# Kernel tuning notes

Measured on AMD Instinct MI355X. Metric: run time of the kernel, lower is better.

## Reference

```python
import jax, jax.numpy as jnp
import numpy as np

NUM_HEADS = 4
NUM_GROUPS = 8
EPS = 1e-5


def group_norm(x, gamma, beta):
    B, C, H, W = x.shape
    xg = x.reshape(B, NUM_GROUPS, C // NUM_GROUPS, H, W)
    mean = xg.mean(axis=(2, 3, 4), keepdims=True)
    var = xg.var(axis=(2, 3, 4), keepdims=True)
    xn = ((xg - mean) * jax.lax.rsqrt(var + EPS)).reshape(B, C, H, W)
    return xn * gamma[None, :, None, None] + beta[None, :, None, None]


def setup_inputs() -> dict:
    key = jax.random.key(0)
    k1, k2, k3 = jax.random.split(key, 3)
    B, C, H, W = 16, 512, 32, 32
    x = jax.random.normal(k1, (B, C, H, W), dtype=jnp.float32)
    gn_gamma = jnp.ones((C,), dtype=jnp.float32)
    gn_beta = jnp.zeros((C,), dtype=jnp.float32)
    w_qkv = jax.random.normal(k2, (3 * C, C), dtype=jnp.float32) * 0.02
    w_proj = jax.random.normal(k3, (C, C), dtype=jnp.float32) * 0.02
    b_proj = jnp.zeros((C,), dtype=jnp.float32)
    return {"x": x, "gn_gamma": gn_gamma, "gn_beta": gn_beta,
            "w_qkv": w_qkv, "w_proj": w_proj, "b_proj": b_proj}


def reference(x, gn_gamma, gn_beta, w_qkv, w_proj, b_proj):
    B, C, H, W = x.shape
    nh = NUM_HEADS
    hd = C // nh
    N = H * W

    x_norm = group_norm(x, gn_gamma, gn_beta)
    # 1x1 conv == channel matmul: (B,C,H,W) x (3C,C) -> (B,3C,H,W)
    qkv = jnp.einsum('bchw,dc->bdhw', x_norm, w_qkv)
    qkv = qkv.reshape(B, 3, nh, hd, N)
    q, k, v = qkv[:, 0], qkv[:, 1], qkv[:, 2]  # each (B, nh, hd, N)

    scale = hd ** (-0.5)
    attn = jnp.einsum('bhci,bhcj->bhij', q, k) * scale  # (B, nh, N, N)
    attn = jax.nn.softmax(attn, axis=-1)
    out = jnp.einsum('bhij,bhcj->bhci', attn, v)  # (B, nh, hd, N)
    out = out.reshape(B, C, H, W)

    proj = jnp.einsum('bchw,dc->bdhw', out, w_proj) + b_proj[None, :, None, None]
    return x + proj
```

## Files before the change

kernel.cpp:

```cpp
#include <hip/hip_runtime.h>
#include <stdint.h>

typedef unsigned char u8;
typedef unsigned short u16;
typedef unsigned int u32;
typedef long long i64;
typedef __attribute__((ext_vector_type(8))) short short8;
typedef __attribute__((ext_vector_type(4))) float f32x4;
typedef __attribute__((ext_vector_type(16))) float f32x16;

#define BATCH 16
#define CCH   512
#define NPIX  1024
#define NGRP  8
#define CPG   64
#define NHEAD 4
#define HDIM  128

__device__ __forceinline__ u16 f2bf(float f) {
  union { float f; u32 u; } v; v.f = f;
  u32 u = v.u;
  u32 r = (u + 0x7FFFu + ((u >> 16) & 1u)) >> 16;
  return (u16)r;
}
__device__ __forceinline__ u8 f2fp8(float f) {
  return (u8)(__builtin_amdgcn_cvt_pk_fp8_f32(f, 0.f, 0, false) & 0xff);
}
__device__ __forceinline__ u32 pack4_fp8(float a, float b, float c, float d) {
  u32 w = (u32)__builtin_amdgcn_cvt_pk_fp8_f32(a, b, 0, false);
  w = (u32)__builtin_amdgcn_cvt_pk_fp8_f32(c, d, (int)w, true);
  return w;
}

__device__ __forceinline__ void gload16(const void* g, void* l) {
  typedef __attribute__((address_space(3))) u32 L;
  typedef __attribute__((address_space(1))) const u32 G;
  __builtin_amdgcn_global_load_lds((G*)(uintptr_t)g, (L*)(u32)(uintptr_t)l, 16, 0, 0);
}

#define PLSWAP(a, b) asm("v_permlane32_swap_b32 %0, %1" : "+v"(a), "+v"(b))

__device__ __forceinline__ short8 rd512(const char* base, int r, int ck, int hi) {
  int byte = ((r >> 2) * 512) +
             ((((r & 3) * 128) + ck * 32 + hi * 16) ^ (((r >> 2) & 15) << 4));
  return *reinterpret_cast<const short8*>(base + byte);
}

__global__ void gn_stats_k(const float* __restrict__ x, float* __restrict__ part) {
  int bg = blockIdx.x >> 3, sl = blockIdx.x & 7;
  const float* p = x + (size_t)bg * (CPG * NPIX) + sl * 8192;
  float s = 0.f, ss = 0.f;
  for (int i = threadIdx.x; i < 2048; i += 256) {
    float4 v = reinterpret_cast<const float4*>(p)[i];
    s  += v.x + v.y + v.z + v.w;
    ss += v.x*v.x + v.y*v.y + v.z*v.z + v.w*v.w;
  }
  for (int o = 32; o > 0; o >>= 1) { s += __shfl_down(s, o); ss += __shfl_down(ss, o); }
  __shared__ float sh[8];
  int wid = threadIdx.x >> 6;
  if ((threadIdx.x & 63) == 0) { sh[wid*2] = s; sh[wid*2+1] = ss; }
  __syncthreads();
  if (threadIdx.x == 0) {
    part[blockIdx.x*2]   = sh[0]+sh[2]+sh[4]+sh[6];
    part[blockIdx.x*2+1] = sh[1]+sh[3]+sh[5]+sh[7];
  }
}

__global__ __launch_bounds__(256) void gn_apply_t(const float* __restrict__ x,
                                                  const float* __restrict__ gamma,
                                                  const float* __restrict__ beta,
                                                  const float* __restrict__ part,
                                                  u16* __restrict__ xnT) {
  const int p0 = blockIdx.x * 64;
  const int c0 = blockIdx.y * 64;
  const int b  = blockIdx.z;
  __shared__ float lt[64][66];

  const int bg = b * NGRP + (c0 >> 6);
  float s = 0.f, ss = 0.f;
  #pragma unroll
  for (int k2 = 0; k2 < 8; ++k2) { s += part[(bg*8 + k2)*2]; ss += part[(bg*8 + k2)*2 + 1]; }
  const float invn = 1.f / (float)(CPG * NPIX);
  const float mean = s * invn;
  const float rstd = rsqrtf(ss * invn - mean * mean + 1e-5f);

  const int t = threadIdx.x;
  #pragma unroll
  for (int pass = 0; pass < 4; ++pass) {
    int c   = c0 + (t >> 4) + pass * 16;
    int pix = p0 + (t & 15) * 4;
    float ga = gamma[c] * rstd;
    float be = beta[c] - mean * ga;
    float4 v = *reinterpret_cast<const float4*>(&x[((size_t)(b*CCH + c)) * NPIX + pix]);
    int pl = (t & 15) * 4, cl = (t >> 4) + pass * 16;
    lt[pl+0][cl] = v.x*ga + be;
    lt[pl+1][cl] = v.y*ga + be;
    lt[pl+2][cl] = v.z*ga + be;
    lt[pl+3][cl] = v.w*ga + be;
  }
  __syncthreads();
  const int pl = t >> 2, cq = (t & 3) * 16;
  u32 wbuf[8];
  #pragma unroll
  for (int e = 0; e < 8; ++e) {
    u16 lo = f2bf(lt[pl][cq + e*2]);
    u16 hi = f2bf(lt[pl][cq + e*2 + 1]);
    wbuf[e] = (u32)lo | ((u32)hi << 16);
  }
  u32* dst = (u32*)&xnT[((size_t)(b*NPIX + p0 + pl)) * CCH + c0 + cq];
  #pragma unroll
  for (int e = 0; e < 8; ++e) dst[e] = wbuf[e];
}

__global__ void f2bf_all(const float* __restrict__ wqkv, const float* __restrict__ wproj,
                         u16* __restrict__ wq, u16* __restrict__ wp) {
  int i = blockIdx.x * 256 + threadIdx.x;
  float4 v; u16* dst;
  if (i < 196608) {
    v = reinterpret_cast<const float4*>(wqkv)[i];
    dst = wq + (size_t)i * 4;
  } else {
    v = reinterpret_cast<const float4*>(wproj)[i - 196608];
    dst = wp + (size_t)(i - 196608) * 4;
  }
  u32 lo = (u32)f2bf(v.x) | ((u32)f2bf(v.y) << 16);
  u32 hi = (u32)f2bf(v.z) | ((u32)f2bf(v.w) << 16);
  *reinterpret_cast<uint2*>(dst) = make_uint2(lo, hi);
}

__global__ __launch_bounds__(256, 2) void gemm_qkv(const u16* __restrict__ xnT,
                                                   const u16* __restrict__ wq_bf,
                                                   u8* __restrict__ outQ,
                                                   u8* __restrict__ outK,
                                                   u8* __restrict__ outV) {
  __shared__ __align__(16) char smem[65536];

  const int id = blockIdx.x;
  const int wg = (id & 7) * 192 + (id >> 3);
  const bool mode0 = (wg < 1024);
  int rt, ct;
  if (mode0) { rt = wg >> 3; ct = wg & 7; }
  else       { int w1 = wg - 1024; rt = w1 & 3; ct = w1 >> 2; }

  const char* Ab = mode0 ? (const char*)xnT + (size_t)rt * 131072
                         : (const char*)wq_bf + (size_t)(8 + rt) * 131072;
  const char* Bb = mode0 ? (const char*)wq_bf + (size_t)ct * 131072
                         : (const char*)xnT + (size_t)ct * 131072;

  const int t = threadIdx.x;
  const int lane = t & 63, w = t >> 6;
  const int q = lane & 31, hi = lane >> 5;
  const int rh = (w >> 1) * 64, ch = (w & 1) * 64;

  int soff[4];
  #pragma unroll
  for (int i = 0; i < 4; ++i) {
    int p = w*4096 + i*1024 + lane*16;
    int lrow = p >> 9, off = p & 511;
    int loff = off ^ ((lrow & 15) << 4);
    soff[i] = (lrow*4 + (loff >> 7)) * 1024 + (loff & 127);
  }

  #pragma unroll
  for (int i = 0; i < 4; ++i) {
    gload16(Ab + soff[i], smem +         w*4096 + i*1024);
    gload16(Bb + soff[i], smem + 16384 + w*4096 + i*1024);
  }

  f32x16 acc[2][2] = {};

  for (int kt = 0; kt < 8; ++kt) {
    asm volatile("s_waitcnt vmcnt(0)" ::: "memory");
    __syncthreads();
    const char* cur = smem + (kt & 1) * 32768;
    if (kt + 1 < 8) {
      char* nxt = smem + ((kt + 1) & 1) * 32768;
      #pragma unroll
      for (int i = 0; i < 4; ++i) {
        gload16(Ab + (kt+1)*128 + soff[i], nxt +         w*4096 + i*1024);
        gload16(Bb + (kt+1)*128 + soff[i], nxt + 16384 + w*4096 + i*1024);
      }
    }
    __builtin_amdgcn_s_setprio(1);
    #pragma unroll
    for (int ck = 0; ck < 4; ++ck) {
      short8 af0 = rd512(cur,         rh + q,      ck, hi);
      short8 af1 = rd512(cur,         rh + 32 + q, ck, hi);
      short8 bf0 = rd512(cur + 16384, ch + q,      ck, hi);
      short8 bf1 = rd512(cur + 16384, ch + 32 + q, ck, hi);
      acc[0][0] = __builtin_amdgcn_mfma_f32_32x32x16_bf16(af0, bf0, acc[0][0], 0, 0, 0);
      acc[0][1] = __builtin_amdgcn_mfma_f32_32x32x16_bf16(af0, bf1, acc[0][1], 0, 0, 0);
      acc[1][0] = __builtin_amdgcn_mfma_f32_32x32x16_bf16(af1, bf0, acc[1][0], 0, 0, 0);
      acc[1][1] = __builtin_amdgcn_mfma_f32_32x32x16_bf16(af1, bf1, acc[1][1], 0, 0, 0);
    }
    __builtin_amdgcn_s_setprio(0);
  }

  __syncthreads();
  u8* Dt = (u8*)smem;
  #pragma unroll
  for (int r = 0; r < 16; ++r) {
    int ar = (r & 3) + 8*(r >> 2) + 4*hi;
    Dt[(rh +      ar) * 144 + ch +      q] = f2fp8(acc[0][0][r]);
    Dt[(rh +      ar) * 144 + ch + 32 + q] = f2fp8(acc[0][1][r]);
    Dt[(rh + 32 + ar) * 144 + ch +      q] = f2fp8(acc[1][0][r]);
    Dt[(rh + 32 + ar) * 144 + ch + 32 + q] = f2fp8(acc[1][1][r]);
  }
  __syncthreads();

  const int rl = t >> 1, hoff = (t & 1) * 64;
  uint4 buf[4];
  const uint4* s4 = reinterpret_cast<const uint4*>(&Dt[rl*144 + hoff]);
  #pragma unroll
  for (int e = 0; e < 4; ++e) buf[e] = s4[e];

  u8* gdst;
  if (mode0) {
    const int tok0 = rt * 128;
    const int b = tok0 >> 10, pix0 = tok0 & 1023;
    const int h = ct & 3;
    u8* base = (ct >= 4) ? outK : outQ;
    gdst = base + ((size_t)((b*NHEAD + h)) * NPIX + pix0 + rl) * HDIM + hoff;
  } else {
    const int m0 = rt * 128, tok0 = ct * 128;
    const int b = tok0 >> 10, pix0 = tok0 & 1023;
    gdst = outV + ((size_t)(b*CCH + m0 + rl)) * NPIX + pix0 + hoff;
  }
  uint4* g4 = reinterpret_cast<uint4*>(gdst);
  #pragma unroll
  for (int e = 0; e < 4; ++e) g4[e] = buf[e];
}

__global__ __launch_bounds__(256, 2) void gemm_proj(const u16* __restrict__ wp_bf,
                                                    const u16* __restrict__ attnO,
                                                    const float* __restrict__ xres,
                                                    const float* __restrict__ bias,
                                                    float* __restrict__ outF) {
  __shared__ __align__(16) char smem[65536];

  const int id = blockIdx.x;
  const int wg = (id & 7) * 64 + (id >> 3);
  const int rt = wg & 3, ct = wg >> 2;

  const char* Ab = (const char*)wp_bf + (size_t)rt * 131072;
  const char* Bb = (const char*)attnO + (size_t)ct * 131072;

  const int t = threadIdx.x;
  const int lane = t & 63, w = t >> 6;
  const int q = lane & 31, hi = lane >> 5;
  const int rh = (w >> 1) * 64, ch = (w & 1) * 64;

  int soff[4];
  #pragma unroll
  for (int i = 0; i < 4; ++i) {
    int p = w*4096 + i*1024 + lane*16;
    int lrow = p >> 9, off = p & 511;
    int loff = off ^ ((lrow & 15) << 4);
    soff[i] = (lrow*4 + (loff >> 7)) * 1024 + (loff & 127);
  }

  #pragma unroll
  for (int i = 0; i < 4; ++i) {
    gload16(Ab + soff[i], smem +         w*4096 + i*1024);
    gload16(Bb + soff[i], smem + 16384 + w*4096 + i*1024);
  }

  f32x16 acc[2][2] = {};

  for (int kt = 0; kt < 8; ++kt) {
    asm volatile("s_waitcnt vmcnt(0)" ::: "memory");
    __syncthreads();
    const char* cur = smem + (kt & 1) * 32768;
    if (kt + 1 < 8) {
      char* nxt = smem + ((kt + 1) & 1) * 32768;
      #pragma unroll
      for (int i = 0; i < 4; ++i) {
        gload16(Ab + (kt+1)*128 + soff[i], nxt +         w*4096 + i*1024);
        gload16(Bb + (kt+1)*128 + soff[i], nxt + 16384 + w*4096 + i*1024);
      }
    }
    __builtin_amdgcn_s_setprio(1);
    #pragma unroll
    for (int ck = 0; ck < 4; ++ck) {
      short8 af0 = rd512(cur,         rh + q,      ck, hi);
      short8 af1 = rd512(cur,         rh + 32 + q, ck, hi);
      short8 bf0 = rd512(cur + 16384, ch + q,      ck, hi);
      short8 bf1 = rd512(cur + 16384, ch + 32 + q, ck, hi);
      acc[0][0] = __builtin_amdgcn_mfma_f32_32x32x16_bf16(af0, bf0, acc[0][0], 0, 0, 0);
      acc[0][1] = __builtin_amdgcn_mfma_f32_32x32x16_bf16(af0, bf1, acc[0][1], 0, 0, 0);
      acc[1][0] = __builtin_amdgcn_mfma_f32_32x32x16_bf16(af1, bf0, acc[1][0], 0, 0, 0);
      acc[1][1] = __builtin_amdgcn_mfma_f32_32x32x16_bf16(af1, bf1, acc[1][1], 0, 0, 0);
    }
    __builtin_amdgcn_s_setprio(0);
  }

  const int m0 = rt * 128, tok0 = ct * 128;
  const int b = tok0 >> 10, pix0 = tok0 & 1023;
  #pragma unroll
  for (int r = 0; r < 16; ++r) {
    int ar = (r & 3) + 8*(r >> 2) + 4*hi;
    int m0r = m0 + rh + ar, m1r = m0 + rh + 32 + ar;
    size_t o00 = ((size_t)(b*CCH + m0r)) * NPIX + pix0 + ch + q;
    size_t o01 = o00 + 32;
    size_t o10 = ((size_t)(b*CCH + m1r)) * NPIX + pix0 + ch + q;
    size_t o11 = o10 + 32;
    outF[o00] = xres[o00] + acc[0][0][r] + bias[m0r];
    outF[o01] = xres[o01] + acc[0][1][r] + bias[m0r];
    outF[o10] = xres[o10] + acc[1][0][r] + bias[m1r];
    outF[o11] = xres[o11] + acc[1][1][r] + bias[m1r];
  }
}

__global__ __launch_bounds__(256, 2) void attn_k(const u8* __restrict__ Qt,
                                                 const u8* __restrict__ Kt,
                                                 const u8* __restrict__ Vb,
                                                 u16* __restrict__ attnO) {
  int id = blockIdx.x;
  int swz = (id & 7) * 64 + (id >> 3);
  const int qt = swz & 7;
  const int h  = (swz >> 3) & 3;
  const int b  = swz >> 5;
  const int bh = b * NHEAD + h;

  __shared__ __align__(16) char smem[32768];

  const int t = threadIdx.x;
  const int lane = t & 63, w = t >> 6;
  const int q = lane & 31, hi = lane >> 5;

  const u8*   Qb    = Qt + ((size_t)bh * NPIX + qt*128 + w*32 + q) * HDIM;
  const char* Kbase = (const char*)Kt + (size_t)bh * NPIX * HDIM;
  const char* Vbase = (const char*)Vb + ((size_t)b*CCH + h*HDIM) * NPIX;

  i64 qf[8];
  #pragma unroll
  for (int ck = 0; ck < 8; ++ck)
    qf[ck] = *reinterpret_cast<const i64*>(Qb + ck*16 + hi*8);

  int koff[2], voff[2];
  #pragma unroll
  for (int i = 0; i < 2; ++i) {
    int d = i*4096 + w*1024 + lane*16;
    int r = d >> 7, x = d & 127;
    koff[i] = r*128 + (x ^ ((r & 15) << 3));
    int vc = 2*r + (x >> 6);
    voff[i] = vc*1024 + ((x & 63) ^ ((r & 7) << 3));
  }

  const int ksw = (q & 15) << 3;

  f32x16 of[4] = {};
  float l_run = 0.f;
  i64 pf[4];
  const float qs2 = 0.08838834764831845f * 1.44269504088896f;

  #pragma unroll
  for (int i = 0; i < 2; ++i)
    gload16(Kbase + koff[i],        smem +        i*4096 + w*1024);
  #pragma unroll
  for (int i = 0; i < 2; ++i)
    gload16(Kbase + 8192 + koff[i], smem + 8192 + i*4096 + w*1024);
  #pragma unroll
  for (int i = 0; i < 2; ++i)
    gload16(Vbase + voff[i],        smem + 16384 + i*4096 + w*1024);
  asm volatile("s_waitcnt vmcnt(0)" ::: "memory");
  __syncthreads();

  {
    f32x16 sn0 = {}, sn1 = {};
    #pragma unroll
    for (int ck = 0; ck < 8; ++ck) {
      const i64 kf0 = *reinterpret_cast<const i64*>(smem + q*128      + ((ck*16 + hi*8) ^ ksw));
      const i64 kf1 = *reinterpret_cast<const i64*>(smem + (32+q)*128 + ((ck*16 + hi*8) ^ ksw));
      sn0 = __builtin_amdgcn_mfma_f32_32x32x16_fp8_fp8(kf0, qf[ck], sn0, 0, 0, 0);
      sn1 = __builtin_amdgcn_mfma_f32_32x32x16_fp8_fp8(kf1, qf[ck], sn1, 0, 0, 0);
    }
    float ps = 0.f;
    float p[16];
    #pragma unroll
    for (int g = 0; g < 2; ++g) {
      const f32x16& sn = g ? sn1 : sn0;
      #pragma unroll
      for (int r = 0; r < 16; ++r) { p[r] = exp2f(sn[r] * qs2); ps += p[r]; }
      u32 pkl0 = pack4_fp8(p[0], p[1], p[2], p[3]);
      u32 pkh0 = pack4_fp8(p[4], p[5], p[6], p[7]);
      u32 pkl1 = pack4_fp8(p[8], p[9], p[10], p[11]);
      u32 pkh1 = pack4_fp8(p[12], p[13], p[14], p[15]);
      PLSWAP(pkl0, pkh0);
      PLSWAP(pkl1, pkh1);
      pf[g*2]   = (i64)(((unsigned long long)pkh0 << 32) | pkl0);
      pf[g*2+1] = (i64)(((unsigned long long)pkh1 << 32) | pkl1);
    }
    ps += __shfl_xor(ps, 32);
    l_run += ps;
  }

  for (int tt = 0; tt < 16; ++tt) {
    asm volatile("s_waitcnt vmcnt(2)" ::: "memory");
    __builtin_amdgcn_s_barrier();

    const char* kcur = smem + (((tt+1) & 1) << 13);
    const char* vcur = smem + 16384 + ((tt & 1) << 13);

    if (tt + 2 < 16) {
      char* kd = smem + ((tt & 1) << 13);
      #pragma unroll
      for (int i = 0; i < 2; ++i)
        gload16(Kbase + (size_t)(tt+2)*8192 + koff[i], kd + i*4096 + w*1024);
    }
    if (tt + 1 < 16) {
      char* vd = smem + 16384 + (((tt+1) & 1) << 13);
      #pragma unroll
      for (int i = 0; i < 2; ++i)
        gload16(Vbase + (size_t)(tt+1)*64 + voff[i], vd + i*4096 + w*1024);
    }

    f32x16 sn0 = {}, sn1 = {};
    __builtin_amdgcn_s_setprio(1);
    if (tt + 1 < 16) {
      #pragma unroll
      for (int ck = 0; ck < 8; ++ck) {
        const i64 kf0 = *reinterpret_cast<const i64*>(kcur + q*128      + ((ck*16 + hi*8) ^ ksw));
        const i64 kf1 = *reinterpret_cast<const i64*>(kcur + (32+q)*128 + ((ck*16 + hi*8) ^ ksw));
        sn0 = __builtin_amdgcn_mfma_f32_32x32x16_fp8_fp8(kf0, qf[ck], sn0, 0, 0, 0);
        sn1 = __builtin_amdgcn_mfma_f32_32x32x16_fp8_fp8(kf1, qf[ck], sn1, 0, 0, 0);
      }
    }
    __builtin_amdgcn_s_setprio(0);

    if (tt < 14)       asm volatile("s_waitcnt vmcnt(4)" ::: "memory");
    else if (tt == 14) asm volatile("s_waitcnt vmcnt(2)" ::: "memory");
    else               asm volatile("s_waitcnt vmcnt(0)" ::: "memory");
    __builtin_amdgcn_s_barrier();

    __builtin_amdgcn_s_setprio(1);
    #pragma unroll
    for (int cg = 0; cg < 4; ++cg) {
      const int c = cg*32 + q;
      const char* vrow = vcur + (c >> 1)*128 + (c & 1)*64;
      const int vsw = ((c >> 1) & 7) << 3;
      #pragma unroll
      for (int kc = 0; kc < 4; ++kc) {
        const i64 vf = *reinterpret_cast<const i64*>(vrow + ((kc*16 + hi*8) ^ vsw));
        of[cg] = __builtin_amdgcn_mfma_f32_32x32x16_fp8_fp8(vf, pf[kc], of[cg], 0, 0, 0);
      }
    }
    __builtin_amdgcn_s_setprio(0);

    if (tt + 1 < 16) {
      float ps = 0.f;
      float p[16];
      #pragma unroll
      for (int g = 0; g < 2; ++g) {
        const f32x16& sn = g ? sn1 : sn0;
        #pragma unroll
        for (int r = 0; r < 16; ++r) { p[r] = exp2f(sn[r] * qs2); ps += p[r]; }
        u32 pkl0 = pack4_fp8(p[0], p[1], p[2], p[3]);
        u32 pkh0 = pack4_fp8(p[4], p[5], p[6], p[7]);
        u32 pkl1 = pack4_fp8(p[8], p[9], p[10], p[11]);
        u32 pkh1 = pack4_fp8(p[12], p[13], p[14], p[15]);
        PLSWAP(pkl0, pkh0);
        PLSWAP(pkl1, pkh1);
        pf[g*2]   = (i64)(((unsigned long long)pkh0 << 32) | pkl0);
        pf[g*2+1] = (i64)(((unsigned long long)pkh1 << 32) | pkl1);
      }
      ps += __shfl_xor(ps, 32);
      l_run += ps;
    }
  }

  float inv = 1.f / l_run;
  u16* orow = attnO + ((size_t)(b*NPIX + qt*128 + w*32 + q)) * CCH + h*HDIM;
  #pragma unroll
  for (int cg = 0; cg < 4; ++cg) {
    #pragma unroll
    for (int u = 0; u < 8; ++u) {
      int c = cg*32 + ((2*u) & 3) + 8*(u >> 1) + 4*hi;
      u32 pk = (u32)f2bf(of[cg][2*u] * inv) | ((u32)f2bf(of[cg][2*u+1] * inv) << 16);
      *reinterpret_cast<u32*>(&orow[c]) = pk;
    }
  }
}

extern "C" void kernel_launch(void* const* d_in, const int* in_sizes, int n_in,
                              void* d_out, int out_size, void* d_ws, size_t ws_size,
                              hipStream_t stream) {
  const float* x     = (const float*)d_in[0];
  const float* gamma = (const float*)d_in[1];
  const float* beta  = (const float*)d_in[2];
  const float* wqkv  = (const float*)d_in[3];
  const float* wproj = (const float*)d_in[4];
  const float* bproj = (const float*)d_in[5];
  float* out = (float*)d_out;

  char* ws = (char*)d_ws;
  float* part   = (float*)ws;
  u16*   xnT    = (u16*)(ws + 8192);
  u16*   wq_bf  = (u16*)(ws + 8192 + (16u<<20));
  u16*   wp_bf  = (u16*)((char*)wq_bf + 1572864);
  u8*    Qt     = (u8*)((char*)wp_bf + 524288);
  u8*    Kt     = (u8*)((char*)Qt + (8u<<20));
  u8*    Vb     = (u8*)((char*)Kt + (8u<<20));
  u16*   attnO  = (u16*)((char*)Vb + (8u<<20));

  gn_stats_k<<<dim3(1024), dim3(256), 0, stream>>>(x, part);
  gn_apply_t<<<dim3(16, 8, BATCH), dim3(256), 0, stream>>>(x, gamma, beta, part, xnT);
  f2bf_all<<<dim3(1024), dim3(256), 0, stream>>>(wqkv, wproj, wq_bf, wp_bf);

  gemm_qkv<<<dim3(1536), dim3(256), 0, stream>>>(xnT, wq_bf, Qt, Kt, Vb);

  attn_k<<<dim3(512), dim3(256), 0, stream>>>(Qt, Kt, Vb, attnO);

  gemm_proj<<<dim3(512), dim3(256), 0, stream>>>(wp_bf, attnO, x, bproj, out);
}
```

Measured before the change: 114.1 us.

## Double attention KV tile to 128 keys and fuse weight conversion into stats kernel

The attention kernel now processes 128 keys per iteration instead of 64, doubling LDS to 64KB, halving the loop trip count and barrier count, and reading V in a new row-swizzled layout. The separate weight fp32-to-bf16 conversion kernel is merged into the group-norm stats kernel as extra blocks, removing one launch. The larger LDS footprint and extra score registers may lower occupancy below the two blocks per CU requested. The new V offset mapping must match how gemm_qkv writes V, and the diff does not show that writer being changed.

```diff
diff --git a/kernel.cpp b/kernel.cpp
--- a/kernel.cpp
+++ b/kernel.cpp
@@ -46,7 +46,25 @@
   return *reinterpret_cast<const short8*>(base + byte);
 }
 
-__global__ void gn_stats_k(const float* __restrict__ x, float* __restrict__ part) {
+__global__ void gn_stats_wconv(const float* __restrict__ x, float* __restrict__ part,
+                               const float* __restrict__ wqkv, const float* __restrict__ wproj,
+                               u16* __restrict__ wq, u16* __restrict__ wp) {
+  __shared__ float sh[8];
+  if (blockIdx.x >= 1024) {
+    int i = (blockIdx.x - 1024) * 256 + threadIdx.x;
+    float4 v; u16* dst;
+    if (i < 196608) {
+      v = reinterpret_cast<const float4*>(wqkv)[i];
+      dst = wq + (size_t)i * 4;
+    } else {
+      v = reinterpret_cast<const float4*>(wproj)[i - 196608];
+      dst = wp + (size_t)(i - 196608) * 4;
+    }
+    u32 lo = (u32)f2bf(v.x) | ((u32)f2bf(v.y) << 16);
+    u32 hi = (u32)f2bf(v.z) | ((u32)f2bf(v.w) << 16);
+    *reinterpret_cast<uint2*>(dst) = make_uint2(lo, hi);
+    return;
+  }
   int bg = blockIdx.x >> 3, sl = blockIdx.x & 7;
   const float* p = x + (size_t)bg * (CPG * NPIX) + sl * 8192;
   float s = 0.f, ss = 0.f;
@@ -56,7 +74,6 @@
     ss += v.x*v.x + v.y*v.y + v.z*v.z + v.w*v.w;
   }
   for (int o = 32; o > 0; o >>= 1) { s += __shfl_down(s, o); ss += __shfl_down(ss, o); }
-  __shared__ float sh[8];
   int wid = threadIdx.x >> 6;
   if ((threadIdx.x & 63) == 0) { sh[wid*2] = s; sh[wid*2+1] = ss; }
   __syncthreads();
@@ -112,22 +129,6 @@
   for (int e = 0; e < 8; ++e) dst[e] = wbuf[e];
 }
 
-__global__ void f2bf_all(const float* __restrict__ wqkv, const float* __restrict__ wproj,
-                         u16* __restrict__ wq, u16* __restrict__ wp) {
-  int i = blockIdx.x * 256 + threadIdx.x;
-  float4 v; u16* dst;
-  if (i < 196608) {
-    v = reinterpret_cast<const float4*>(wqkv)[i];
-    dst = wq + (size_t)i * 4;
-  } else {
-    v = reinterpret_cast<const float4*>(wproj)[i - 196608];
-    dst = wp + (size_t)(i - 196608) * 4;
-  }
-  u32 lo = (u32)f2bf(v.x) | ((u32)f2bf(v.y) << 16);
-  u32 hi = (u32)f2bf(v.z) | ((u32)f2bf(v.w) << 16);
-  *reinterpret_cast<uint2*>(dst) = make_uint2(lo, hi);
-}
-
 __global__ __launch_bounds__(256, 2) void gemm_qkv(const u16* __restrict__ xnT,
                                                    const u16* __restrict__ wq_bf,
                                                    u8* __restrict__ outQ,
@@ -322,7 +323,7 @@
   const int b  = swz >> 5;
   const int bh = b * NHEAD + h;
 
-  __shared__ __align__(16) char smem[32768];
+  __shared__ __align__(16) char smem[65536];
 
   const int t = threadIdx.x;
   const int lane = t & 63, w = t >> 6;
@@ -337,132 +338,147 @@
   for (int ck = 0; ck < 8; ++ck)
     qf[ck] = *reinterpret_cast<const i64*>(Qb + ck*16 + hi*8);
 
-  int koff[2], voff[2];
-  #pragma unroll
-  for (int i = 0; i < 2; ++i) {
+  int koff[4], voff[4];
+  #pragma unroll
+  for (int i = 0; i < 4; ++i) {
     int d = i*4096 + w*1024 + lane*16;
     int r = d >> 7, x = d & 127;
     koff[i] = r*128 + (x ^ ((r & 15) << 3));
-    int vc = 2*r + (x >> 6);
-    voff[i] = vc*1024 + ((x & 63) ^ ((r & 7) << 3));
+    voff[i] = r*1024 + (x ^ ((r & 15) << 3));
   }
 
   const int ksw = (q & 15) << 3;
 
   f32x16 of[4] = {};
   float l_run = 0.f;
-  i64 pf[4];
+  i64 pf[8];
   const float qs2 = 0.08838834764831845f * 1.44269504088896f;
 
   #pragma unroll
-  for (int i = 0; i < 2; ++i)
-    gload16(Kbase + koff[i],        smem +        i*4096 + w*1024);
-  #pragma unroll
-  for (int i = 0; i < 2; ++i)
-    gload16(Kbase + 8192 + koff[i], smem + 8192 + i*4096 + w*1024);
-  #pragma unroll
-  for (int i = 0; i < 2; ++i)
-    gload16(Vbase + voff[i],        smem + 16384 + i*4096 + w*1024);
+  for (int i = 0; i < 4; ++i)
+    gload16(Kbase + koff[i],         smem +         i*4096 + w*1024);
+  #pragma unroll
+  for (int i = 0; i < 4; ++i)
+    gload16(Kbase + 16384 + koff[i], smem + 16384 + i*4096 + w*1024);
+  #pragma unroll
+  for (int i = 0; i < 4; ++i)
+    gload16(Vbase + voff[i],         smem + 32768 + i*4096 + w*1024);
   asm volatile("s_waitcnt vmcnt(0)" ::: "memory");
   __syncthreads();
 
   {
-    f32x16 sn0 = {}, sn1 = {};
+    f32x16 sn0 = {}, sn1 = {}, sn2 = {}, sn3 = {};
     #pragma unroll
     for (int ck = 0; ck < 8; ++ck) {
-      const i64 kf0 = *reinterpret_cast<const i64*>(smem + q*128      + ((ck*16 + hi*8) ^ ksw));
-      const i64 kf1 = *reinterpret_cast<const i64*>(smem + (32+q)*128 + ((ck*16 + hi*8) ^ ksw));
+      const int co = (ck*16 + hi*8) ^ ksw;
+      const i64 kf0 = *reinterpret_cast<const i64*>(smem + (q)*128      + co);
+      const i64 kf1 = *reinterpret_cast<const i64*>(smem + (32+q)*128   + co);
+      const i64 kf2 = *reinterpret_cast<const i64*>(smem + (64+q)*128   + co);
+      const i64 kf3 = *reinterpret_cast<const i64*>(smem + (96+q)*128   + co);
       sn0 = __builtin_amdgcn_mfma_f32_32x32x16_fp8_fp8(kf0, qf[ck], sn0, 0, 0, 0);
       sn1 = __builtin_amdgcn_mfma_f32_32x32x16_fp8_fp8(kf1, qf[ck], sn1, 0, 0, 0);
+      sn2 = __builtin_amdgcn_mfma_f32_32x32x16_fp8_fp8(kf2, qf[ck], sn2, 0, 0, 0);
+      sn3 = __builtin_amdgcn_mfma_f32_32x32x16_fp8_fp8(kf3, qf[ck], sn3, 0, 0, 0);
     }
     float ps = 0.f;
-    float p[16];
     #pragma unroll
-    for (int g = 0; g < 2; ++g) {
-      const f32x16& sn = g ? sn1 : sn0;
-      #pragma unroll
-      for (int r = 0; r < 16; ++r) { p[r] = exp2f(sn[r] * qs2); ps += p[r]; }
-      u32 pkl0 = pack4_fp8(p[0], p[1], p[2], p[3]);
-      u32 pkh0 = pack4_fp8(p[4], p[5], p[6], p[7]);
-      u32 pkl1 = pack4_fp8(p[8], p[9], p[10], p[11]);
-      u32 pkh1 = pack4_fp8(p[12], p[13], p[14], p[15]);
-      PLSWAP(pkl0, pkh0);
-      PLSWAP(pkl1, pkh1);
-      pf[g*2]   = (i64)(((unsigned long long)pkh0 << 32) | pkl0);
-      pf[g*2+1] = (i64)(((unsigned long long)pkh1 << 32) | pkl1);
+    for (int g = 0; g < 4; ++g) {
+      const f32x16& sn = (g == 0) ? sn0 : (g == 1) ? sn1 : (g == 2) ? sn2 : sn3;
+      float p[16];
+      float psa = 0.f, psb = 0.f;
+      #pragma unroll
+      for (int r = 0; r < 8; ++r)  { p[r] = exp2f(sn[r] * qs2); psa += p[r]; }
+      #pragma unroll
+      for (int r = 8; r < 16; ++r) { p[r] = exp2f(sn[r] * qs2); psb += p[r]; }
+      u32 w0 = pack4_fp8(p[0], p[1], p[2], p[3]);
+      u32 w1 = pack4_fp8(p[4], p[5], p[6], p[7]);
+      u32 w2 = pack4_fp8(p[8], p[9], p[10], p[11]);
+      u32 w3 = pack4_fp8(p[12], p[13], p[14], p[15]);
+      PLSWAP(w0, w1);
+      PLSWAP(w2, w3);
+      pf[g*2]   = (i64)(((unsigned long long)w1 << 32) | w0);
+      pf[g*2+1] = (i64)(((unsigned long long)w3 << 32) | w2);
+      ps += psa + psb;
     }
     ps += __shfl_xor(ps, 32);
     l_run += ps;
   }
 
-  for (int tt = 0; tt < 16; ++tt) {
-    asm volatile("s_waitcnt vmcnt(2)" ::: "memory");
+  for (int tt = 0; tt < 8; ++tt) {
+    asm volatile("s_waitcnt vmcnt(4)" ::: "memory");
     __builtin_amdgcn_s_barrier();
 
-    const char* kcur = smem + (((tt+1) & 1) << 13);
-    const char* vcur = smem + 16384 + ((tt & 1) << 13);
-
-    if (tt + 2 < 16) {
-      char* kd = smem + ((tt & 1) << 13);
-      #pragma unroll
-      for (int i = 0; i < 2; ++i)
-        gload16(Kbase + (size_t)(tt+2)*8192 + koff[i], kd + i*4096 + w*1024);
-    }
-    if (tt + 1 < 16) {
-      char* vd = smem + 16384 + (((tt+1) & 1) << 13);
-      #pragma unroll
-      for (int i = 0; i < 2; ++i)
-        gload16(Vbase + (size_t)(tt+1)*64 + voff[i], vd + i*4096 + w*1024);
-    }
-
-    f32x16 sn0 = {}, sn1 = {};
+    const char* kcur = smem + (((tt+1) & 1) << 14);
+    const char* vcur = smem + 32768 + ((tt & 1) << 14);
+
+    if (tt + 2 < 8) {
+      char* kd = smem + ((tt & 1) << 14);
+      #pragma unroll
+      for (int i = 0; i < 4; ++i)
+        gload16(Kbase + (size_t)(tt+2)*16384 + koff[i], kd + i*4096 + w*1024);
+    }
+    if (tt + 1 < 8) {
+      char* vd = smem + 32768 + (((tt+1) & 1) << 14);
+      #pragma unroll
+      for (int i = 0; i < 4; ++i)
+        gload16(Vbase + (size_t)(tt+1)*128 + voff[i], vd + i*4096 + w*1024);
+    }
+
+    f32x16 sn0 = {}, sn1 = {}, sn2 = {}, sn3 = {};
     __builtin_amdgcn_s_setprio(1);
-    if (tt + 1 < 16) {
+    if (tt + 1 < 8) {
       #pragma unroll
       for (int ck = 0; ck < 8; ++ck) {
-        const i64 kf0 = *reinterpret_cast<const i64*>(kcur + q*128      + ((ck*16 + hi*8) ^ ksw));
-        const i64 kf1 = *reinterpret_cast<const i64*>(kcur + (32+q)*128 + ((ck*16 + hi*8) ^ ksw));
+        const int co = (ck*16 + hi*8) ^ ksw;
+        const i64 kf0 = *reinterpret_cast<const i64*>(kcur + (q)*128    + co);
+        const i64 kf1 = *reinterpret_cast<const i64*>(kcur + (32+q)*128 + co);
+        const i64 kf2 = *reinterpret_cast<const i64*>(kcur + (64+q)*128 + co);
+        const i64 kf3 = *reinterpret_cast<const i64*>(kcur + (96+q)*128 + co);
         sn0 = __builtin_amdgcn_mfma_f32_32x32x16_fp8_fp8(kf0, qf[ck], sn0, 0, 0, 0);
         sn1 = __builtin_amdgcn_mfma_f32_32x32x16_fp8_fp8(kf1, qf[ck], sn1, 0, 0, 0);
+        sn2 = __builtin_amdgcn_mfma_f32_32x32x16_fp8_fp8(kf2, qf[ck], sn2, 0, 0, 0);
+        sn3 = __builtin_amdgcn_mfma_f32_32x32x16_fp8_fp8(kf3, qf[ck], sn3, 0, 0, 0);
       }
     }
     __builtin_amdgcn_s_setprio(0);
 
-    if (tt < 14)       asm volatile("s_waitcnt vmcnt(4)" ::: "memory");
-    else if (tt == 14) asm volatile("s_waitcnt vmcnt(2)" ::: "memory");
-    else               asm volatile("s_waitcnt vmcnt(0)" ::: "memory");
+    if (tt < 6)       asm volatile("s_waitcnt vmcnt(8)" ::: "memory");
+    else if (tt == 6) asm volatile("s_waitcnt vmcnt(4)" ::: "memory");
+    else              asm volatile("s_waitcnt vmcnt(0)" ::: "memory");
     __builtin_amdgcn_s_barrier();
 
     __builtin_amdgcn_s_setprio(1);
     #pragma unroll
     for (int cg = 0; cg < 4; ++cg) {
-      const int c = cg*32 + q;
-      const char* vrow = vcur + (c >> 1)*128 + (c & 1)*64;
-      const int vsw = ((c >> 1) & 7) << 3;
-      #pragma unroll
-      for (int kc = 0; kc < 4; ++kc) {
-        const i64 vf = *reinterpret_cast<const i64*>(vrow + ((kc*16 + hi*8) ^ vsw));
+      const char* vrow = vcur + (cg*32 + q)*128;
+      #pragma unroll
+      for (int kc = 0; kc < 8; ++kc) {
+        const i64 vf = *reinterpret_cast<const i64*>(vrow + ((kc*16 + hi*8) ^ ksw));
         of[cg] = __builtin_amdgcn_mfma_f32_32x32x16_fp8_fp8(vf, pf[kc], of[cg], 0, 0, 0);
       }
     }
     __builtin_amdgcn_s_setprio(0);
 
-    if (tt + 1 < 16) {
+    if (tt + 1 < 8) {
       float ps = 0.f;
-      float p[16];
-      #pragma unroll
-      for (int g = 0; g < 2; ++g) {
-        const f32x16& sn = g ? sn1 : sn0;
+      #pragma unroll
+      for (int g = 0; g < 4; ++g) {
+        const f32x16& sn = (g == 0) ? sn0 : (g == 1) ? sn1 : (g == 2) ? sn2 : sn3;
+        float p[16];
+        float psa = 0.f, psb = 0.f;
         #pragma unroll
-        for (int r = 0; r < 16; ++r) { p[r] = exp2f(sn[r] * qs2); ps += p[r]; }
-        u32 pkl0 = pack4_fp8(p[0], p[1], p[2], p[3]);
-        u32 pkh0 = pack4_fp8(p[4], p[5], p[6], p[7]);
-        u32 pkl1 = pack4_fp8(p[8], p[9], p[10], p[11]);
-        u32 pkh1 = pack4_fp8(p[12], p[13], p[14], p[15]);
-        PLSWAP(pkl0, pkh0);
-        PLSWAP(pkl1, pkh1);
-        pf[g*2]   = (i64)(((unsigned long long)pkh0 << 32) | pkl0);
-        pf[g*2+1] = (i64)(((unsigned long long)pkh1 << 32) | pkl1);
+        for (int r = 0; r < 8; ++r)  { p[r] = exp2f(sn[r] * qs2); psa += p[r]; }
+        #pragma unroll
+        for (int r = 8; r < 16; ++r) { p[r] = exp2f(sn[r] * qs2); psb += p[r]; }
+        u32 w0 = pack4_fp8(p[0], p[1], p[2], p[3]);
+        u32 w1 = pack4_fp8(p[4], p[5], p[6], p[7]);
+        u32 w2 = pack4_fp8(p[8], p[9], p[10], p[11]);
+        u32 w3 = pack4_fp8(p[12], p[13], p[14], p[15]);
+        PLSWAP(w0, w1);
+        PLSWAP(w2, w3);
+        pf[g*2]   = (i64)(((unsigned long long)w1 << 32) | w0);
+        pf[g*2+1] = (i64)(((unsigned long long)w3 << 32) | w2);
+        ps += psa + psb;
       }
       ps += __shfl_xor(ps, 32);
       l_run += ps;
@@ -503,9 +519,8 @@
   u8*    Vb     = (u8*)((char*)Kt + (8u<<20));
   u16*   attnO  = (u16*)((char*)Vb + (8u<<20));
 
-  gn_stats_k<<<dim3(1024), dim3(256), 0, stream>>>(x, part);
+  gn_stats_wconv<<<dim3(2048), dim3(256), 0, stream>>>(x, part, wqkv, wproj, wq_bf, wp_bf);
   gn_apply_t<<<dim3(16, 8, BATCH), dim3(256), 0, stream>>>(x, gamma, beta, part, xnT);
-  f2bf_all<<<dim3(1024), dim3(256), 0, stream>>>(wqkv, wproj, wq_bf, wp_bf);
 
   gemm_qkv<<<dim3(1536), dim3(256), 0, stream>>>(xnT, wq_bf, Qt, Kt, Vb);
 
```

Measured after the change: 110.9 us, median of 2. 1.03x faster.
